# Kernel optimization log

Hardware: AMD Instinct MI355X
Metric: run time of the kernel (lower is better)

Reference implementation:

```python
import jax, jax.numpy as jnp
import numpy as np
from jax import lax

EPS = 1e-5

def haar_dwt(x):
    # pywt 'haar' dwt2: a=(x0+x1)/sqrt2, d=(x0-x1)/sqrt2 per axis
    B, C, H, W = x.shape
    xr = x.reshape(B, C, H // 2, 2, W // 2, 2)
    x00 = xr[:, :, :, 0, :, 0]; x01 = xr[:, :, :, 0, :, 1]
    x10 = xr[:, :, :, 1, :, 0]; x11 = xr[:, :, :, 1, :, 1]
    ll = (x00 + x01 + x10 + x11) * 0.5
    lh = (x00 + x01 - x10 - x11) * 0.5  # cH: detail along rows
    hl = (x00 - x01 + x10 - x11) * 0.5  # cV: detail along cols
    hh = (x00 - x01 - x10 + x11) * 0.5  # cD
    return ll, lh, hl, hh

def haar_idwt(ll, lh, hl, hh):
    y00 = (ll + lh + hl + hh) * 0.5
    y01 = (ll + lh - hl - hh) * 0.5
    y10 = (ll - lh + hl - hh) * 0.5
    y11 = (ll - lh - hl + hh) * 0.5
    B, C, H, W = ll.shape
    top = jnp.stack([y00, y01], axis=-1)      # [B,C,H,W,2]
    bot = jnp.stack([y10, y11], axis=-1)
    y = jnp.stack([top, bot], axis=3)          # [B,C,H,2,W,2]
    return y.reshape(B, C, 2 * H, 2 * W)

def conv1x1(x, w, b):
    # w: [Cout, Cin]
    return jnp.einsum('bchw,oc->bohw', x, w) + b[None, :, None, None]

def batchnorm(x, g, b):
    mu = jnp.mean(x, axis=(0, 2, 3), keepdims=True)
    var = jnp.var(x, axis=(0, 2, 3), keepdims=True)
    xh = (x - mu) * lax.rsqrt(var + EPS)
    return xh * g[None, :, None, None] + b[None, :, None, None]

def layernorm_chw(x, g, b):
    # GroupNorm(1, C): normalize over (C,H,W) per sample
    mu = jnp.mean(x, axis=(1, 2, 3), keepdims=True)
    var = jnp.var(x, axis=(1, 2, 3), keepdims=True)
    xh = (x - mu) * lax.rsqrt(var + EPS)
    return xh * g[None, :, None, None] + b[None, :, None, None]

def dwconv3x3(x, w, b):
    # w: [C,1,3,3] depthwise
    C = x.shape[1]
    y = lax.conv_general_dilated(x, w, (1, 1), [(1, 1), (1, 1)],
                                 dimension_numbers=('NCHW', 'OIHW', 'NCHW'),
                                 feature_group_count=C)
    return y + b[None, :, None, None]

gelu = lambda x: jax.nn.gelu(x, approximate=False)

def setup_inputs() -> dict:
    key = jax.random.key(0)
    ks = jax.random.split(key, 16)
    C = 128
    B, H, W = 8, 256, 256
    f = jnp.float32
    s = lambda k, shape, fan: jax.random.normal(k, shape, f) * (1.0 / np.sqrt(fan))
    return {
        'x': jax.random.normal(ks[0], (B, C, H, W), f),
        'w_c1': s(ks[1], (C, 4 * C), 4 * C), 'b_c1': jnp.zeros((C,), f),
        'bn1_g': jnp.ones((C,), f), 'bn1_b': jnp.zeros((C,), f),
        'dw_w': s(ks[2], (C, 1, 3, 3), 9), 'dw_b': jnp.zeros((C,), f),
        'gn_g': jnp.ones((C,), f), 'gn_b': jnp.zeros((C,), f),
        'pw1_w': s(ks[3], (C, C), C), 'pw1_b': jnp.zeros((C,), f),
        'pw2_w': s(ks[4], (C, C), C), 'pw2_b': jnp.zeros((C,), f),
        'w_c2': s(ks[5], (4 * C, C), C), 'b_c2': jnp.zeros((4 * C,), f),
        'bn2_g': jnp.ones((4 * C,), f), 'bn2_b': jnp.zeros((4 * C,), f),
    }

def reference(x, w_c1, b_c1, bn1_g, bn1_b, dw_w, dw_b, gn_g, gn_b,
              pw1_w, pw1_b, pw2_w, pw2_b, w_c2, b_c2, bn2_g, bn2_b):
    ll, lh, hl, hh = haar_dwt(x)
    h = jnp.concatenate([ll, lh, hl, hh], axis=1)       # [B,4C,H/2,W/2]
    h = gelu(batchnorm(conv1x1(h, w_c1, b_c1), bn1_g, bn1_b))
    # BasicBlock
    res = h
    o = dwconv3x3(h, dw_w, dw_b)
    o = layernorm_chw(o, gn_g, gn_b)
    o = conv1x1(o, pw1_w, pw1_b)
    o = gelu(o)
    o = conv1x1(o, pw2_w, pw2_b)
    h = o + res
    h = gelu(batchnorm(conv1x1(h, w_c2, b_c2), bn2_g, bn2_b))
    C = h.shape[1] // 4
    return haar_idwt(h[:, :C], h[:, C:2 * C], h[:, 2 * C:3 * C], h[:, 3 * C:])
```

## Files before the change

kernel.cpp:

```cpp
#include <hip/hip_runtime.h>
#include <hip/hip_bf16.h>

typedef unsigned short u16;
typedef unsigned int u32;
typedef __attribute__((ext_vector_type(8))) short short8;
typedef __attribute__((ext_vector_type(4))) float f32x4;

#define Bq 8
#define Cc 128
#define C4 512
#define Hh 256
#define Wf 256
#define H2 128
#define W2 128
#define HW2 16384
#define NPIX 131072.0f

__device__ __forceinline__ float gelu_f(float x) {
    float u = 1.5957691216057308f * (x + 0.044715f * x * x * x);
    float t = 1.0f - 2.0f / (__expf(u) + 1.0f);
    return 0.5f * x * (1.0f + t);
}
__device__ __forceinline__ float bf2f(u16 u) {
    union { float f; u32 i; } v; v.i = ((u32)u) << 16; return v.f;
}
__device__ __forceinline__ u16 f2bf(float f) {
    union { float f; u32 i; } v; v.f = f;
    u32 r = v.i + 0x7FFFu + ((v.i >> 16) & 1u);
    return (u16)(r >> 16);
}

__global__ __launch_bounds__(256) void k_wconv(const float* __restrict__ w_c1,
                                               const float* __restrict__ pw1,
                                               const float* __restrict__ pw2,
                                               const float* __restrict__ w_c2,
                                               const float* __restrict__ gn_g,
                                               u16* __restrict__ wb) {
    int i = blockIdx.x * 256 + threadIdx.x;
    float v;
    if (i < 65536) {
        int o = i >> 9, kn = i & 511;
        int c = kn >> 2, dy = (kn >> 1) & 1, dx = kn & 1;
        float sdy = dy ? -1.f : 1.f, sdx = dx ? -1.f : 1.f;
        const float* wr = w_c1 + o * 512 + c;
        v = 0.5f * (wr[0] + sdy * wr[128] + sdx * wr[256] + sdy * sdx * wr[384]);
    } else if (i < 81920) v = pw1[i - 65536] * gn_g[(i - 65536) & 127];
    else if (i < 98304) v = pw2[i - 81920];
    else v = w_c2[i - 98304];
    wb[i] = f2bf(v);
}

__global__ __launch_bounds__(128) void k_wvec(const float* __restrict__ pw1,
                                              const float* __restrict__ gg,
                                              const float* __restrict__ gb,
                                              float* __restrict__ wbv,
                                              float* __restrict__ wgs) {
    int o = threadIdx.x;
    float a = 0.f, bv = 0.f;
    for (int c = 0; c < 128; ++c) {
        float w = pw1[o * 128 + c];
        a += w * gg[c];
        bv += w * gb[c];
    }
    wgs[o] = a;
    wbv[o] = bv;
}

__global__ __launch_bounds__(512) void k_conv1(const float* __restrict__ x,
                                               const u16* __restrict__ Wt,
                                               u16* __restrict__ Cout,
                                               float* __restrict__ statS,
                                               float* __restrict__ statQ) {
    __shared__ __align__(16) u16 lds[16384];
    __shared__ float sblk[128], qblk[128];
    const int t = threadIdx.x;
    const int lane = t & 63, w = t >> 6, wr = w & 1, wc = w >> 1;
    const int b = blockIdx.z, i = blockIdx.y;
    if (t < 128) { sblk[t] = 0.f; qblk[t] = 0.f; }

    const int r15 = lane & 15, kq = lane >> 4;
    const int half = t >> 8;
    const int colblk = t & 7, cc = (t >> 3) & 15, dy = (t >> 7) & 1;
    const int kbase = cc * 4 + dy * 2;
    const int gG = kbase >> 3, e2 = (kbase & 7) * 2;

    float4 xv[4];
    uint4 rb[2];
    {
        const float* xp = x + (((long)(b * Cc + cc)) * Hh + (2 * i + dy)) * Wf;
#pragma unroll
        for (int q = 0; q < 4; ++q) {
            int col = (half * 4 + q) * 32 + colblk * 4;
            xv[q] = *(const float4*)(xp + col);
        }
#pragma unroll
        for (int ii = 0; ii < 2; ++ii) {
            int s = ii * 512 + t;
            rb[ii] = *(const uint4*)(Wt + (long)(s >> 3) * 512 + (s & 7) * 8);
        }
    }

    f32x4 acc[4][2];
#pragma unroll
    for (int a2 = 0; a2 < 4; ++a2)
#pragma unroll
        for (int j2 = 0; j2 < 2; ++j2) acc[a2][j2] = (f32x4){0.f, 0.f, 0.f, 0.f};

    for (int k0 = 0; k0 < 512; k0 += 64) {
        __syncthreads();
#pragma unroll
        for (int q = 0; q < 4; ++q) {
            int col = (half * 4 + q) * 32 + colblk * 4;
            int j0 = col >> 1;
            u32 p0 = (u32)f2bf(xv[q].x) | ((u32)f2bf(xv[q].y) << 16);
            u32 p1 = (u32)f2bf(xv[q].z) | ((u32)f2bf(xv[q].w) << 16);
            *(u32*)((char*)lds + j0 * 128 + 16 * (gG ^ (j0 & 7)) + e2) = p0;
            *(u32*)((char*)lds + (j0 + 1) * 128 + 16 * (gG ^ ((j0 + 1) & 7)) + e2) = p1;
        }
#pragma unroll
        for (int ii = 0; ii < 2; ++ii) {
            int s = ii * 512 + t;
            int row_ = s >> 3, ch_ = s & 7;
            *(uint4*)((char*)lds + 16384 + row_ * 128 + 16 * (ch_ ^ (row_ & 7))) = rb[ii];
        }
        __syncthreads();
        if (k0 + 64 < 512) {
            const int c0n = (k0 + 64) >> 2;
            const float* xp = x + (((long)(b * Cc + c0n + cc)) * Hh + (2 * i + dy)) * Wf;
#pragma unroll
            for (int q = 0; q < 4; ++q) {
                int col = (half * 4 + q) * 32 + colblk * 4;
                xv[q] = *(const float4*)(xp + col);
            }
#pragma unroll
            for (int ii = 0; ii < 2; ++ii) {
                int s = ii * 512 + t;
                rb[ii] = *(const uint4*)(Wt + (long)(s >> 3) * 512 + (k0 + 64) + (s & 7) * 8);
            }
        }
#pragma unroll
        for (int ks = 0; ks < 2; ++ks) {
            short8 af[4], bfv[2];
            const int ch = ks * 4 + kq;
#pragma unroll
            for (int mi = 0; mi < 4; ++mi) {
                int row = wr * 64 + mi * 16 + r15;
                af[mi] = *(const short8*)((const char*)lds + row * 128 + 16 * (ch ^ (row & 7)));
            }
#pragma unroll
            for (int ni = 0; ni < 2; ++ni) {
                int row = wc * 32 + ni * 16 + r15;
                bfv[ni] = *(const short8*)((const char*)lds + 16384 + row * 128 + 16 * (ch ^ (row & 7)));
            }
#pragma unroll
            for (int mi = 0; mi < 4; ++mi)
#pragma unroll
                for (int ni = 0; ni < 2; ++ni)
                    acc[mi][ni] = __builtin_amdgcn_mfma_f32_16x16x32_bf16(
                        af[mi], bfv[ni], acc[mi][ni], 0, 0, 0);
        }
    }
    __syncthreads();

#pragma unroll
    for (int mi = 0; mi < 4; ++mi)
#pragma unroll
        for (int ni = 0; ni < 2; ++ni)
#pragma unroll
            for (int r = 0; r < 4; ++r) {
                int row = wr * 64 + mi * 16 + kq * 4 + r;
                int col = wc * 32 + ni * 16 + r15;
                lds[row * 128 + (col ^ ((row & 7) << 3))] = f2bf(acc[mi][ni][r]);
            }
#pragma unroll
    for (int ni = 0; ni < 2; ++ni) {
        float s = 0.f, q2 = 0.f;
#pragma unroll
        for (int mi = 0; mi < 4; ++mi)
#pragma unroll
            for (int r = 0; r < 4; ++r) {
                float v = acc[mi][ni][r];
                s += v; q2 += v * v;
            }
        s += __shfl_down(s, 32); s += __shfl_down(s, 16);
        q2 += __shfl_down(q2, 32); q2 += __shfl_down(q2, 16);
        if (lane < 16) {
            int col = wc * 32 + ni * 16 + r15;
            atomicAdd(&sblk[col], s);
            atomicAdd(&qblk[col], q2);
        }
    }
    __syncthreads();
    {
        u16* Cb = Cout + (long)b * HW2 * 128;
        int row = t >> 2, quarter = (t & 3) * 32;
        int sx = (row & 7) << 3;
        long gbase = (long)(i * 128 + row) * 128;
#pragma unroll
        for (int q = 0; q < 4; ++q) {
            int c = quarter + q * 8;
            *(uint4*)(Cb + gbase + c) = *(const uint4*)(lds + row * 128 + (c ^ sx));
        }
    }
    if (t < 128) {
        atomicAdd(statS + (long)t * 16, sblk[t]);
        atomicAdd(statQ + (long)t * 16, qblk[t]);
    }
}

__global__ __launch_bounds__(256) void k_bn1_gelu(const u16* __restrict__ in,
                                                  u16* __restrict__ out,
                                                  const float* __restrict__ sum,
                                                  const float* __restrict__ sq,
                                                  const float* __restrict__ g,
                                                  const float* __restrict__ bb) {
    long e = ((long)blockIdx.x * 256 + threadIdx.x) * 8;
    int c0 = (int)(e & 127);
    uint4 raw = *(const uint4*)(in + e);
    u16* pv = (u16*)&raw;
    const float invN = 1.0f / 131072.0f;
#pragma unroll
    for (int u = 0; u < 8; ++u) {
        int c = c0 + u;
        float mu = sum[(long)c * 16] * invN;
        float var = sq[(long)c * 16] * invN - mu * mu;
        float rscale = rsqrtf(var + 1e-5f);
        float sc = rscale * g[c], sh = bb[c] - mu * sc;
        pv[u] = f2bf(gelu_f(bf2f(pv[u]) * sc + sh));
    }
    *(uint4*)(out + e) = raw;
}

__global__ __launch_bounds__(256) void k_dwconv(const u16* __restrict__ x,
                                                u16* __restrict__ y,
                                                const float* __restrict__ w,
                                                const float* __restrict__ bias,
                                                float* __restrict__ lnS,
                                                float* __restrict__ lnQ) {
    __shared__ float wl2[1152];
    const int t = threadIdx.x;
    for (int idx = t; idx < 1152; idx += 256) {
        int c = idx / 9, tap = idx - c * 9;
        wl2[tap * 128 + (c & 7) * 16 + (c >> 3)] = w[idx];
    }
    __syncthreads();
    const int cg = t & 15, jj = t >> 4;
    const int j = blockIdx.x * 16 + jj, i = blockIdx.y, b = blockIdx.z;
    const u16* xb = x + (long)b * HW2 * 128 + cg * 8;
    uint4 raw[3][3];
    const uint4 z4 = make_uint4(0u, 0u, 0u, 0u);
#pragma unroll
    for (int r = 0; r < 3; ++r) {
        int row = i - 1 + r;
#pragma unroll
        for (int q = 0; q < 3; ++q) {
            int col = j - 1 + q;
            bool ok = (row >= 0) & (row < H2) & (col >= 0) & (col < W2);
            raw[r][q] = ok ? *(const uint4*)(xb + ((long)row * W2 + col) * 128) : z4;
        }
    }
    float acc[8];
#pragma unroll
    for (int u = 0; u < 8; ++u) acc[u] = bias[cg * 8 + u];
#pragma unroll
    for (int r = 0; r < 3; ++r)
#pragma unroll
        for (int q = 0; q < 3; ++q) {
            const u16* pv = (const u16*)&raw[r][q];
            const int tap = r * 3 + q;
#pragma unroll
            for (int u = 0; u < 8; ++u)
                acc[u] = fmaf(bf2f(pv[u]), wl2[tap * 128 + u * 16 + cg], acc[u]);
        }
    uint4 outv; u16* ov = (u16*)&outv;
    float s = 0.f, q2 = 0.f;
#pragma unroll
    for (int u = 0; u < 8; ++u) {
        ov[u] = f2bf(acc[u]);
        s += acc[u]; q2 += acc[u] * acc[u];
    }
    *(uint4*)(y + ((long)b * HW2 + (long)i * W2 + j) * 128 + cg * 8) = outv;
#pragma unroll
    for (int off = 32; off; off >>= 1) {
        s += __shfl_down(s, off);
        q2 += __shfl_down(q2, off);
    }
    __shared__ float r1[4], r2[4];
    if ((t & 63) == 0) { r1[t >> 6] = s; r2[t >> 6] = q2; }
    __syncthreads();
    if (t == 0) {
        int slot = (blockIdx.y * 8 + blockIdx.x) & 63;
        atomicAdd(lnS + ((long)b * 64 + slot) * 16, r1[0] + r1[1] + r1[2] + r1[3]);
        atomicAdd(lnQ + ((long)b * 64 + slot) * 16, r2[0] + r2[1] + r2[2] + r2[3]);
    }
}

__global__ __launch_bounds__(256) void k_mlp(const u16* __restrict__ D,
                                             const u16* __restrict__ Wp1,
                                             const u16* __restrict__ Wp2,
                                             const float* __restrict__ b1,
                                             const float* __restrict__ b2,
                                             const u16* __restrict__ resH,
                                             u16* __restrict__ Yout,
                                             const float* __restrict__ lnS,
                                             const float* __restrict__ lnQ,
                                             const float* __restrict__ wbv,
                                             const float* __restrict__ wgs) {
    __shared__ __align__(16) u16 lA[16384];
    __shared__ __align__(16) u16 lB[16384];
    __shared__ float s1[128], s2[128], lnred[2];
    const int t = threadIdx.x;
    const int lane = t & 63, w = t >> 6, wr = w >> 1, wc = w & 1;
    const int r15 = lane & 15, kq = lane >> 4;
    const int b = blockIdx.z, m0 = blockIdx.y * 128;

    if (t < 64) {
        float s = lnS[((long)b * 64 + t) * 16];
        float q = lnQ[((long)b * 64 + t) * 16];
#pragma unroll
        for (int off = 32; off; off >>= 1) {
            s += __shfl_down(s, off);
            q += __shfl_down(q, off);
        }
        if (t == 0) { lnred[0] = s; lnred[1] = q; }
    }
    __syncthreads();
    const float invN = 1.0f / 2097152.0f;
    float mu = lnred[0] * invN;
    float var = lnred[1] * invN - mu * mu;
    const float rs = rsqrtf(var + 1e-5f);
    if (t < 128) {
        s1[t] = b1[t] + wbv[t] - mu * rs * wgs[t];
        s2[t] = b2[t];
    }

    const u16* Ab = D + ((long)b * HW2 + m0) * 128;
    uint4 ga[8], gb[8];
#pragma unroll
    for (int i = 0; i < 8; ++i) {
        int s = i * 256 + t, row = s >> 4, seg = s & 15;
        ga[i] = *(const uint4*)(Ab + (long)row * 128 + seg * 8);
        gb[i] = *(const uint4*)(Wp1 + (long)row * 128 + seg * 8);
    }
#pragma unroll
    for (int i = 0; i < 8; ++i) {
        int s = i * 256 + t, row = s >> 4, seg = s & 15;
        int off = (seg >> 3) * 16384 + row * 128 + 16 * ((seg & 7) ^ (row & 7));
        *(uint4*)((char*)lA + off) = ga[i];
        *(uint4*)((char*)lB + off) = gb[i];
    }
    __syncthreads();

    f32x4 acc[4][4];
#pragma unroll
    for (int i = 0; i < 4; ++i)
#pragma unroll
        for (int j = 0; j < 4; ++j) acc[i][j] = (f32x4){0.f, 0.f, 0.f, 0.f};
#pragma unroll
    for (int chunk = 0; chunk < 2; ++chunk)
#pragma unroll
        for (int ks = 0; ks < 2; ++ks) {
            const int ch = ks * 4 + kq;
            short8 af[4], bfv[4];
#pragma unroll
            for (int mi = 0; mi < 4; ++mi) {
                int row = wr * 64 + mi * 16 + r15;
                af[mi] = *(const short8*)((const char*)lA + chunk * 16384 +
                                          row * 128 + 16 * (ch ^ (row & 7)));
            }
#pragma unroll
            for (int ni = 0; ni < 4; ++ni) {
                int row = wc * 64 + ni * 16 + r15;
                bfv[ni] = *(const short8*)((const char*)lB + chunk * 16384 +
                                           row * 128 + 16 * (ch ^ (row & 7)));
            }
#pragma unroll
            for (int mi = 0; mi < 4; ++mi)
#pragma unroll
                for (int ni = 0; ni < 4; ++ni)
                    acc[mi][ni] = __builtin_amdgcn_mfma_f32_16x16x32_bf16(
                        af[mi], bfv[ni], acc[mi][ni], 0, 0, 0);
        }
#pragma unroll
    for (int i = 0; i < 8; ++i) {
        int s = i * 256 + t, row = s >> 4, seg = s & 15;
        gb[i] = *(const uint4*)(Wp2 + (long)row * 128 + seg * 8);
    }
    __syncthreads();

#pragma unroll
    for (int mi = 0; mi < 4; ++mi)
#pragma unroll
        for (int ni = 0; ni < 4; ++ni)
#pragma unroll
            for (int r = 0; r < 4; ++r) {
                int row = wr * 64 + mi * 16 + kq * 4 + r;
                int col = wc * 64 + ni * 16 + r15;
                float v = gelu_f(rs * acc[mi][ni][r] + s1[col]);
                lA[(col >> 6) * 8192 + row * 64 +
                   8 * (((col >> 3) & 7) ^ (row & 7)) + (col & 7)] = f2bf(v);
            }
#pragma unroll
    for (int i = 0; i < 8; ++i) {
        int s = i * 256 + t, row = s >> 4, seg = s & 15;
        int off = (seg >> 3) * 16384 + row * 128 + 16 * ((seg & 7) ^ (row & 7));
        *(uint4*)((char*)lB + off) = gb[i];
    }
    __syncthreads();

#pragma unroll
    for (int i = 0; i < 4; ++i)
#pragma unroll
        for (int j = 0; j < 4; ++j) acc[i][j] = (f32x4){0.f, 0.f, 0.f, 0.f};
#pragma unroll
    for (int chunk = 0; chunk < 2; ++chunk)
#pragma unroll
        for (int ks = 0; ks < 2; ++ks) {
            const int ch = ks * 4 + kq;
            short8 af[4], bfv[4];
#pragma unroll
            for (int mi = 0; mi < 4; ++mi) {
                int row = wr * 64 + mi * 16 + r15;
                af[mi] = *(const short8*)((const char*)lA + chunk * 16384 +
                                          row * 128 + 16 * (ch ^ (row & 7)));
            }
#pragma unroll
            for (int ni = 0; ni < 4; ++ni) {
                int row = wc * 64 + ni * 16 + r15;
                bfv[ni] = *(const short8*)((const char*)lB + chunk * 16384 +
                                           row * 128 + 16 * (ch ^ (row & 7)));
            }
#pragma unroll
            for (int mi = 0; mi < 4; ++mi)
#pragma unroll
                for (int ni = 0; ni < 4; ++ni)
                    acc[mi][ni] = __builtin_amdgcn_mfma_f32_16x16x32_bf16(
                        af[mi], bfv[ni], acc[mi][ni], 0, 0, 0);
        }
    __syncthreads();

#pragma unroll
    for (int mi = 0; mi < 4; ++mi)
#pragma unroll
        for (int ni = 0; ni < 4; ++ni)
#pragma unroll
            for (int r = 0; r < 4; ++r) {
                int row = wr * 64 + mi * 16 + kq * 4 + r;
                int col = wc * 64 + ni * 16 + r15;
                lA[row * 128 + (col ^ ((row & 7) << 3))] = f2bf(acc[mi][ni][r]);
            }
    __syncthreads();

    const u16* Rb = resH + ((long)b * HW2 + m0) * 128;
    u16* Cb = Yout + ((long)b * HW2 + m0) * 128;
    {
        int row = t >> 1, half = (t & 1) * 64;
        int sx = (row & 7) << 3;
#pragma unroll
        for (int q = 0; q < 8; ++q) {
            int c = half + q * 8;
            uint4 raw = *(const uint4*)(lA + row * 128 + (c ^ sx));
            uint4 rr = *(const uint4*)(Rb + (long)row * 128 + c);
            u16* pv = (u16*)&raw;
            const u16* rv = (const u16*)&rr;
#pragma unroll
            for (int u = 0; u < 8; ++u)
                pv[u] = f2bf(bf2f(pv[u]) + s2[c + u] + bf2f(rv[u]));
            *(uint4*)(Cb + (long)row * 128 + c) = raw;
        }
    }
}

__global__ __launch_bounds__(256) void k_moment(const u16* __restrict__ Y,
                                                float* __restrict__ M2,
                                                float* __restrict__ csum) {
    __shared__ __align__(16) u16 T[8192];
    __shared__ float cred[16][16][8];
    const int t = threadIdx.x;
    const int lane = t & 63, w = t >> 6, wr = w >> 1, wc = w & 1;
    const int r15 = lane & 15, kq = lane >> 4;
    const long px0 = (long)blockIdx.x * 1024;
    float cs[8] = {};

    f32x4 acc[4][4];
#pragma unroll
    for (int i = 0; i < 4; ++i)
#pragma unroll
        for (int j = 0; j < 4; ++j) acc[i][j] = (f32x4){0.f, 0.f, 0.f, 0.f};

    for (int it = 0; it < 16; ++it) {
        uint4 rv[4];
#pragma unroll
        for (int i = 0; i < 4; ++i) {
            int s = i * 256 + t;
            int px = s >> 4, ch8 = (s & 15) * 8;
            rv[i] = *(const uint4*)(Y + (px0 + it * 64 + px) * 128 + ch8);
        }
#pragma unroll
        for (int i = 0; i < 4; ++i) {
            const u16* pv = (const u16*)&rv[i];
#pragma unroll
            for (int u = 0; u < 8; ++u) cs[u] += bf2f(pv[u]);
        }
        __syncthreads();
#pragma unroll
        for (int i = 0; i < 4; ++i) {
            int s = i * 256 + t;
            int px = s >> 4, ch8 = (s & 15) * 8;
            const u16* pv = (const u16*)&rv[i];
#pragma unroll
            for (int u = 0; u < 8; ++u) {
                int row = ch8 + u;
                T[row * 64 + 8 * ((px >> 3) ^ (row & 7)) + (px & 7)] = pv[u];
            }
        }
        __syncthreads();
#pragma unroll
        for (int ks = 0; ks < 2; ++ks) {
            const int ch = ks * 4 + kq;
            short8 af[4], bfv[4];
#pragma unroll
            for (int mi = 0; mi < 4; ++mi) {
                int row = wr * 64 + mi * 16 + r15;
                af[mi] = *(const short8*)(T + row * 64 + 8 * (ch ^ (row & 7)));
            }
#pragma unroll
            for (int ni = 0; ni < 4; ++ni) {
                int row = wc * 64 + ni * 16 + r15;
                bfv[ni] = *(const short8*)(T + row * 64 + 8 * (ch ^ (row & 7)));
            }
#pragma unroll
            for (int mi = 0; mi < 4; ++mi)
#pragma unroll
                for (int ni = 0; ni < 4; ++ni)
                    acc[mi][ni] = __builtin_amdgcn_mfma_f32_16x16x32_bf16(
                        af[mi], bfv[ni], acc[mi][ni], 0, 0, 0);
        }
    }
    {
        int g = t & 15, m = t >> 4;
#pragma unroll
        for (int u = 0; u < 8; ++u) cred[m][g][u] = cs[u];
    }
    __syncthreads();
    if (t < 128) {
        float s = 0.f;
#pragma unroll
        for (int m = 0; m < 16; ++m) s += cred[m][t >> 3][t & 7];
        atomicAdd(csum + (long)t * 16, s);
    }
#pragma unroll
    for (int mi = 0; mi < 4; ++mi)
#pragma unroll
        for (int ni = 0; ni < 4; ++ni)
#pragma unroll
            for (int r = 0; r < 4; ++r) {
                int row = wr * 64 + mi * 16 + kq * 4 + r;
                int col = wc * 64 + ni * 16 + r15;
                atomicAdd(M2 + row * 128 + col, acc[mi][ni][r]);
            }
}

__global__ __launch_bounds__(128) void k_statcomb(const float* __restrict__ w_c2,
                                                  const float* __restrict__ M2,
                                                  const float* __restrict__ csum,
                                                  const float* __restrict__ g,
                                                  const float* __restrict__ bb,
                                                  float* __restrict__ scsh) {
    __shared__ float wl[128];
    __shared__ float red[2][2];
    const int o = blockIdx.x, c = threadIdx.x;
    wl[c] = w_c2[o * 128 + c];
    __syncthreads();
    const float* m2r = M2 + c * 128;
    float tmp = 0.f;
#pragma unroll
    for (int c2 = 0; c2 < 128; c2 += 4) {
        float4 m = *(const float4*)(m2r + c2);
        tmp += m.x * wl[c2] + m.y * wl[c2 + 1] + m.z * wl[c2 + 2] + m.w * wl[c2 + 3];
    }
    float s2p = wl[c] * tmp;
    float mup = wl[c] * csum[(long)c * 16];
#pragma unroll
    for (int off = 32; off; off >>= 1) {
        s2p += __shfl_down(s2p, off);
        mup += __shfl_down(mup, off);
    }
    if ((c & 63) == 0) { red[0][c >> 6] = s2p; red[1][c >> 6] = mup; }
    __syncthreads();
    if (c == 0) {
        float s2 = (red[0][0] + red[0][1]) / NPIX;
        float mu = (red[1][0] + red[1][1]) / NPIX;
        float var = s2 - mu * mu;
        float rs = rsqrtf(var + 1e-5f);
        float sc = g[o] * rs;
        scsh[o] = sc;
        scsh[512 + o] = bb[o] - mu * sc;
    }
}

__global__ __launch_bounds__(512) void k_conv2_idwt(const u16* __restrict__ Y,
                                                    const u16* __restrict__ Wc,
                                                    const float* __restrict__ scsh,
                                                    float* __restrict__ out) {
    __shared__ __align__(16) u16 lA[16384];
    __shared__ __align__(16) u16 lB[8192];
    __shared__ float sparam[1024];
    const int t = threadIdx.x;
    const int lane = t & 63, w = t >> 6, wr = w & 1, wc = w >> 1;
    const int r15 = lane & 15, kq = lane >> 4;
    const int b = blockIdx.y, n0 = blockIdx.x;
#pragma unroll
    for (int u = 0; u < 2; ++u) sparam[t + u * 512] = scsh[t + u * 512];

    const u16* Yb = Y + ((long)b * HW2 + (long)n0 * 64) * 128;
    uint4 rb2[2], ra4[4];
#pragma unroll
    for (int i = 0; i < 2; ++i) {
        int s = i * 512 + t, row = s >> 4, seg = s & 15;
        rb2[i] = *(const uint4*)(Yb + (long)row * 128 + seg * 8);
    }
#define GLOADA(q)                                                                \
    {                                                                            \
        _Pragma("unroll")                                                        \
        for (int i = 0; i < 4; ++i) {                                            \
            int s = i * 512 + t, row = s >> 4, seg = s & 15;                     \
            ra4[i] = *(const uint4*)(Wc + (long)((q) * 128 + row) * 128 + seg * 8); \
        }                                                                        \
    }
#define LWRITEA()                                                                \
    {                                                                            \
        _Pragma("unroll")                                                        \
        for (int i = 0; i < 4; ++i) {                                            \
            int s = i * 512 + t, row = s >> 4, seg = s & 15;                     \
            *(uint4*)((char*)lA + (seg >> 3) * 16384 + row * 128 +               \
                      16 * ((seg & 7) ^ (row & 7))) = ra4[i];                    \
        }                                                                        \
    }
    GLOADA(0)
#pragma unroll
    for (int i = 0; i < 2; ++i) {
        int s = i * 512 + t, row = s >> 4, seg = s & 15;
        *(uint4*)((char*)lB + (seg >> 3) * 8192 + row * 128 +
                  16 * ((seg & 7) ^ (row & 7))) = rb2[i];
    }
    LWRITEA()
    __syncthreads();

    u32 sbp[4][4][2];
#pragma unroll
    for (int q = 0; q < 4; ++q) {
        f32x4 acc[4];
#pragma unroll
        for (int mi = 0; mi < 4; ++mi) acc[mi] = (f32x4){0.f, 0.f, 0.f, 0.f};
#pragma unroll
        for (int chunk = 0; chunk < 2; ++chunk)
#pragma unroll
            for (int ks = 0; ks < 2; ++ks) {
                const int ch = ks * 4 + kq;
                short8 af[4], bfv;
#pragma unroll
                for (int mi = 0; mi < 4; ++mi) {
                    int row = wr * 64 + mi * 16 + r15;
                    af[mi] = *(const short8*)((const char*)lA + chunk * 16384 +
                                              row * 128 + 16 * (ch ^ (row & 7)));
                }
                {
                    int row = wc * 16 + r15;
                    bfv = *(const short8*)((const char*)lB + chunk * 8192 +
                                           row * 128 + 16 * (ch ^ (row & 7)));
                }
#pragma unroll
                for (int mi = 0; mi < 4; ++mi)
                    acc[mi] = __builtin_amdgcn_mfma_f32_16x16x32_bf16(
                        af[mi], bfv, acc[mi], 0, 0, 0);
            }
        if (q < 3) GLOADA(q + 1)
#pragma unroll
        for (int mi = 0; mi < 4; ++mi)
#pragma unroll
            for (int rp = 0; rp < 2; ++rp) {
                int c0 = q * 128 + wr * 64 + mi * 16 + kq * 4 + rp * 2;
                float v0 = gelu_f(acc[mi][rp * 2] * sparam[c0] + sparam[512 + c0]);
                float v1 = gelu_f(acc[mi][rp * 2 + 1] * sparam[c0 + 1] + sparam[512 + c0 + 1]);
                sbp[q][mi][rp] = (u32)f2bf(v0) | ((u32)f2bf(v1) << 16);
            }
        if (q < 3) {
            __syncthreads();
            LWRITEA()
            __syncthreads();
        }
    }
    const int i = n0 >> 1;
    const int j = (n0 & 1) * 64 + wc * 16 + r15;
#pragma unroll
    for (int mi = 0; mi < 4; ++mi)
#pragma unroll
        for (int rp = 0; rp < 2; ++rp) {
            u32 p0 = sbp[0][mi][rp], p1 = sbp[1][mi][rp];
            u32 p2 = sbp[2][mi][rp], p3 = sbp[3][mi][rp];
#pragma unroll
            for (int e = 0; e < 2; ++e) {
                int c = wr * 64 + mi * 16 + kq * 4 + rp * 2 + e;
                float ll = bf2f(e ? (u16)(p0 >> 16) : (u16)(p0 & 0xFFFF));
                float lh = bf2f(e ? (u16)(p1 >> 16) : (u16)(p1 & 0xFFFF));
                float hl = bf2f(e ? (u16)(p2 >> 16) : (u16)(p2 & 0xFFFF));
                float hh = bf2f(e ? (u16)(p3 >> 16) : (u16)(p3 & 0xFFFF));
                long ob = (((long)(b * Cc + c) * Hh + 2 * i) * Wf + 2 * j);
                *(float2*)(out + ob) =
                    make_float2((ll + lh + hl + hh) * 0.5f, (ll + lh - hl - hh) * 0.5f);
                *(float2*)(out + ob + Wf) =
                    make_float2((ll - lh + hl - hh) * 0.5f, (ll - lh - hl + hh) * 0.5f);
            }
        }
#undef GLOADA
#undef LWRITEA
}

extern "C" void kernel_launch(void* const* d_in, const int* in_sizes, int n_in,
                              void* d_out, int out_size, void* d_ws, size_t ws_size,
                              hipStream_t stream) {
    const float* x     = (const float*)d_in[0];
    const float* w_c1  = (const float*)d_in[1];
    const float* bn1_g = (const float*)d_in[3];
    const float* bn1_b = (const float*)d_in[4];
    const float* dw_w  = (const float*)d_in[5];
    const float* dw_b  = (const float*)d_in[6];
    const float* gn_g  = (const float*)d_in[7];
    const float* gn_b  = (const float*)d_in[8];
    const float* pw1_w = (const float*)d_in[9];
    const float* pw1_b = (const float*)d_in[10];
    const float* pw2_w = (const float*)d_in[11];
    const float* pw2_b = (const float*)d_in[12];
    const float* w_c2  = (const float*)d_in[13];
    const float* bn2_g = (const float*)d_in[15];
    const float* bn2_b = (const float*)d_in[16];
    float* out = (float*)d_out;

    const size_t n128 = (size_t)Bq * Cc * HW2;
    u16* bufA = (u16*)d_ws;
    u16* bufH = bufA + n128;
    u16* bufD = bufH + n128;
    u16* bufY = bufD + n128;
    u16* wb   = bufY + n128;
    float* stats = (float*)(wb + 163840);
    size_t need = (4 * n128 + 163840) * 2 + 41000 * 4;
    if (ws_size < need) return;

    float* bn1_sum = stats;
    float* bn1_sq  = stats + 2048;
    float* ln_sum  = stats + 4096;
    float* ln_sq   = stats + 12288;
    float* csum    = stats + 20480;
    float* M2      = stats + 22528;
    float* scsh    = stats + 38912;
    float* wbv     = stats + 39936;
    float* wgs     = stats + 40064;

    hipMemsetAsync(stats, 0, 38912 * sizeof(float), stream);

    k_wconv<<<640, 256, 0, stream>>>(w_c1, pw1_w, pw2_w, w_c2, gn_g, wb);
    k_wvec<<<1, 128, 0, stream>>>(pw1_w, gn_g, gn_b, wbv, wgs);

    k_conv1<<<dim3(1, 128, 8), 512, 0, stream>>>(x, wb, bufA, bn1_sum, bn1_sq);

    k_bn1_gelu<<<8192, 256, 0, stream>>>(bufA, bufH, bn1_sum, bn1_sq, bn1_g, bn1_b);

    k_dwconv<<<dim3(8, 128, 8), 256, 0, stream>>>(bufH, bufD, dw_w, dw_b, ln_sum, ln_sq);

    k_mlp<<<dim3(1, 128, 8), 256, 0, stream>>>(
        bufD, wb + 65536, wb + 81920, pw1_b, pw2_b, bufH, bufY,
        ln_sum, ln_sq, wbv, wgs);

    k_moment<<<128, 256, 0, stream>>>(bufY, M2, csum);
    k_statcomb<<<512, 128, 0, stream>>>(w_c2, M2, csum, bn2_g, bn2_b, scsh);

    k_conv2_idwt<<<dim3(256, 8), 512, 0, stream>>>(bufY, wb + 98304, scsh, out);
}
```

Baseline: 476.5 us.

## Fuse BN1+GELU into dwconv and MLP residual; replace M2 atomics with partial reduction

Removes the standalone BN1+GELU pass. The depthwise conv now stages a halo tile in LDS and applies the BN scale/shift plus GELU while loading it. The MLP kernel recomputes GELU(BN(x)) for its residual input, which removes one full bf16 tensor write and read. The moment kernel now writes per-block partial Gram matrices, and a new reduction kernel sums them instead of issuing global float atomics. The costs are recomputed GELU work, a larger workspace for the partials (about 8 MB), and an extra kernel launch.

```diff
diff --git a/kernel.cpp b/kernel.cpp
--- a/kernel.cpp
+++ b/kernel.cpp
@@ -208,69 +208,73 @@
     }
 }
 
-__global__ __launch_bounds__(256) void k_bn1_gelu(const u16* __restrict__ in,
-                                                  u16* __restrict__ out,
-                                                  const float* __restrict__ sum,
-                                                  const float* __restrict__ sq,
-                                                  const float* __restrict__ g,
-                                                  const float* __restrict__ bb) {
-    long e = ((long)blockIdx.x * 256 + threadIdx.x) * 8;
-    int c0 = (int)(e & 127);
-    uint4 raw = *(const uint4*)(in + e);
-    u16* pv = (u16*)&raw;
-    const float invN = 1.0f / 131072.0f;
-#pragma unroll
-    for (int u = 0; u < 8; ++u) {
-        int c = c0 + u;
-        float mu = sum[(long)c * 16] * invN;
-        float var = sq[(long)c * 16] * invN - mu * mu;
-        float rscale = rsqrtf(var + 1e-5f);
-        float sc = rscale * g[c], sh = bb[c] - mu * sc;
-        pv[u] = f2bf(gelu_f(bf2f(pv[u]) * sc + sh));
-    }
-    *(uint4*)(out + e) = raw;
-}
-
-__global__ __launch_bounds__(256) void k_dwconv(const u16* __restrict__ x,
+__global__ __launch_bounds__(256) void k_dwconv(const u16* __restrict__ xin,
                                                 u16* __restrict__ y,
                                                 const float* __restrict__ w,
                                                 const float* __restrict__ bias,
+                                                const float* __restrict__ bnS,
+                                                const float* __restrict__ bnQ,
+                                                const float* __restrict__ g1,
+                                                const float* __restrict__ b1,
                                                 float* __restrict__ lnS,
                                                 float* __restrict__ lnQ) {
     __shared__ float wl2[1152];
+    __shared__ float sA[128], sB[128];
+    __shared__ __align__(16) u16 tile[3 * 18 * 136];
     const int t = threadIdx.x;
+    if (t < 128) {
+        const float invN = 1.0f / 131072.0f;
+        float mu = bnS[(long)t * 16] * invN;
+        float var = bnQ[(long)t * 16] * invN - mu * mu;
+        float rs = rsqrtf(var + 1e-5f);
+        float sc = rs * g1[t];
+        sA[t] = sc;
+        sB[t] = b1[t] - mu * sc;
+    }
     for (int idx = t; idx < 1152; idx += 256) {
         int c = idx / 9, tap = idx - c * 9;
         wl2[tap * 128 + (c & 7) * 16 + (c >> 3)] = w[idx];
     }
     __syncthreads();
+    const int jbase = blockIdx.x * 16, i = blockIdx.y, b = blockIdx.z;
+    const u16* xb = xin + (long)b * HW2 * 128;
+    {
+        int seg = t & 15, slot0 = t >> 4;
+#pragma unroll
+        for (int pass = 0; pass < 4; ++pass) {
+            int slot = pass * 16 + slot0;
+            if (slot < 54) {
+                int r = slot / 18, p = slot - r * 18;
+                int row = i - 1 + r, col = jbase - 1 + p;
+                bool inb = (row >= 0) & (row < H2) & (col >= 0) & (col < W2);
+                uint4 raw = inb ? *(const uint4*)(xb + ((long)row * W2 + col) * 128 + seg * 8)
+                                : make_uint4(0u, 0u, 0u, 0u);
+                const u16* pv = (const u16*)&raw;
+                uint4 outv; u16* ov = (u16*)&outv;
+#pragma unroll
+                for (int u = 0; u < 8; ++u) {
+                    int c = seg * 8 + u;
+                    float v = inb ? gelu_f(bf2f(pv[u]) * sA[c] + sB[c]) : 0.f;
+                    ov[u] = f2bf(v);
+                }
+                *(uint4*)(tile + slot * 136 + seg * 8) = outv;
+            }
+        }
+    }
+    __syncthreads();
     const int cg = t & 15, jj = t >> 4;
-    const int j = blockIdx.x * 16 + jj, i = blockIdx.y, b = blockIdx.z;
-    const u16* xb = x + (long)b * HW2 * 128 + cg * 8;
-    uint4 raw[3][3];
-    const uint4 z4 = make_uint4(0u, 0u, 0u, 0u);
-#pragma unroll
-    for (int r = 0; r < 3; ++r) {
-        int row = i - 1 + r;
-#pragma unroll
-        for (int q = 0; q < 3; ++q) {
-            int col = j - 1 + q;
-            bool ok = (row >= 0) & (row < H2) & (col >= 0) & (col < W2);
-            raw[r][q] = ok ? *(const uint4*)(xb + ((long)row * W2 + col) * 128) : z4;
-        }
-    }
     float acc[8];
 #pragma unroll
     for (int u = 0; u < 8; ++u) acc[u] = bias[cg * 8 + u];
 #pragma unroll
     for (int r = 0; r < 3; ++r)
 #pragma unroll
-        for (int q = 0; q < 3; ++q) {
-            const u16* pv = (const u16*)&raw[r][q];
-            const int tap = r * 3 + q;
+        for (int dj = 0; dj < 3; ++dj) {
+            short8 vv = *(const short8*)(tile + (r * 18 + jj + dj) * 136 + cg * 8);
+            const int tap = r * 3 + dj;
 #pragma unroll
             for (int u = 0; u < 8; ++u)
-                acc[u] = fmaf(bf2f(pv[u]), wl2[tap * 128 + u * 16 + cg], acc[u]);
+                acc[u] = fmaf(bf2f((u16)vv[u]), wl2[tap * 128 + u * 16 + cg], acc[u]);
         }
     uint4 outv; u16* ov = (u16*)&outv;
     float s = 0.f, q2 = 0.f;
@@ -279,7 +283,7 @@
         ov[u] = f2bf(acc[u]);
         s += acc[u]; q2 += acc[u] * acc[u];
     }
-    *(uint4*)(y + ((long)b * HW2 + (long)i * W2 + j) * 128 + cg * 8) = outv;
+    *(uint4*)(y + ((long)b * HW2 + (long)i * W2 + jbase + jj) * 128 + cg * 8) = outv;
 #pragma unroll
     for (int off = 32; off; off >>= 1) {
         s += __shfl_down(s, off);
@@ -298,17 +302,21 @@
 __global__ __launch_bounds__(256) void k_mlp(const u16* __restrict__ D,
                                              const u16* __restrict__ Wp1,
                                              const u16* __restrict__ Wp2,
-                                             const float* __restrict__ b1,
-                                             const float* __restrict__ b2,
-                                             const u16* __restrict__ resH,
+                                             const float* __restrict__ b1p,
+                                             const float* __restrict__ b2p,
+                                             const u16* __restrict__ resA,
                                              u16* __restrict__ Yout,
                                              const float* __restrict__ lnS,
                                              const float* __restrict__ lnQ,
                                              const float* __restrict__ wbv,
-                                             const float* __restrict__ wgs) {
+                                             const float* __restrict__ wgs,
+                                             const float* __restrict__ bnS,
+                                             const float* __restrict__ bnQ,
+                                             const float* __restrict__ g1,
+                                             const float* __restrict__ b1v) {
     __shared__ __align__(16) u16 lA[16384];
     __shared__ __align__(16) u16 lB[16384];
-    __shared__ float s1[128], s2[128], lnred[2];
+    __shared__ float s1[128], s2[128], sA[128], sB[128], lnred[2];
     const int t = threadIdx.x;
     const int lane = t & 63, w = t >> 6, wr = w >> 1, wc = w & 1;
     const int r15 = lane & 15, kq = lane >> 4;
@@ -330,8 +338,15 @@
     float var = lnred[1] * invN - mu * mu;
     const float rs = rsqrtf(var + 1e-5f);
     if (t < 128) {
-        s1[t] = b1[t] + wbv[t] - mu * rs * wgs[t];
-        s2[t] = b2[t];
+        s1[t] = b1p[t] + wbv[t] - mu * rs * wgs[t];
+        s2[t] = b2p[t];
+        const float invN1 = 1.0f / 131072.0f;
+        float mu1 = bnS[(long)t * 16] * invN1;
+        float var1 = bnQ[(long)t * 16] * invN1 - mu1 * mu1;
+        float rs1 = rsqrtf(var1 + 1e-5f);
+        float sc1 = rs1 * g1[t];
+        sA[t] = sc1;
+        sB[t] = b1v[t] - mu1 * sc1;
     }
 
     const u16* Ab = D + ((long)b * HW2 + m0) * 128;
@@ -451,7 +466,7 @@
             }
     __syncthreads();
 
-    const u16* Rb = resH + ((long)b * HW2 + m0) * 128;
+    const u16* Ra = resA + ((long)b * HW2 + m0) * 128;
     u16* Cb = Yout + ((long)b * HW2 + m0) * 128;
     {
         int row = t >> 1, half = (t & 1) * 64;
@@ -460,19 +475,21 @@
         for (int q = 0; q < 8; ++q) {
             int c = half + q * 8;
             uint4 raw = *(const uint4*)(lA + row * 128 + (c ^ sx));
-            uint4 rr = *(const uint4*)(Rb + (long)row * 128 + c);
+            uint4 rr = *(const uint4*)(Ra + (long)row * 128 + c);
             u16* pv = (u16*)&raw;
             const u16* rv = (const u16*)&rr;
 #pragma unroll
-            for (int u = 0; u < 8; ++u)
-                pv[u] = f2bf(bf2f(pv[u]) + s2[c + u] + bf2f(rv[u]));
+            for (int u = 0; u < 8; ++u) {
+                float hres = gelu_f(bf2f(rv[u]) * sA[c + u] + sB[c + u]);
+                pv[u] = f2bf(bf2f(pv[u]) + s2[c + u] + hres);
+            }
             *(uint4*)(Cb + (long)row * 128 + c) = raw;
         }
     }
 }
 
 __global__ __launch_bounds__(256) void k_moment(const u16* __restrict__ Y,
-                                                float* __restrict__ M2,
+                                                float* __restrict__ M2p,
                                                 float* __restrict__ csum) {
     __shared__ __align__(16) u16 T[8192];
     __shared__ float cred[16][16][8];
@@ -549,6 +566,7 @@
         for (int m = 0; m < 16; ++m) s += cred[m][t >> 3][t & 7];
         atomicAdd(csum + (long)t * 16, s);
     }
+    float* Mb = M2p + (long)blockIdx.x * 16384;
 #pragma unroll
     for (int mi = 0; mi < 4; ++mi)
 #pragma unroll
@@ -557,8 +575,16 @@
             for (int r = 0; r < 4; ++r) {
                 int row = wr * 64 + mi * 16 + kq * 4 + r;
                 int col = wc * 64 + ni * 16 + r15;
-                atomicAdd(M2 + row * 128 + col, acc[mi][ni][r]);
-            }
+                Mb[row * 128 + col] = acc[mi][ni][r];
+            }
+}
+
+__global__ __launch_bounds__(256) void k_m2red(const float* __restrict__ M2p,
+                                               float* __restrict__ M2) {
+    int e = blockIdx.x * 256 + threadIdx.x;
+    float s = 0.f;
+    for (int p = 0; p < 128; ++p) s += M2p[(long)p * 16384 + e];
+    M2[e] = s;
 }
 
 __global__ __launch_bounds__(128) void k_statcomb(const float* __restrict__ w_c2,
@@ -739,12 +765,12 @@
 
     const size_t n128 = (size_t)Bq * Cc * HW2;
     u16* bufA = (u16*)d_ws;
-    u16* bufH = bufA + n128;
-    u16* bufD = bufH + n128;
+    u16* bufD = bufA + n128;
     u16* bufY = bufD + n128;
     u16* wb   = bufY + n128;
     float* stats = (float*)(wb + 163840);
-    size_t need = (4 * n128 + 163840) * 2 + 41000 * 4;
+    float* M2p = stats + 49152;
+    size_t need = (3 * n128 + 163840) * 2 + (49152 + 128 * 16384) * 4;
     if (ws_size < need) return;
 
     float* bn1_sum = stats;
@@ -757,22 +783,23 @@
     float* wbv     = stats + 39936;
     float* wgs     = stats + 40064;
 
-    hipMemsetAsync(stats, 0, 38912 * sizeof(float), stream);
+    hipMemsetAsync(stats, 0, 22528 * sizeof(float), stream);
 
     k_wconv<<<640, 256, 0, stream>>>(w_c1, pw1_w, pw2_w, w_c2, gn_g, wb);
     k_wvec<<<1, 128, 0, stream>>>(pw1_w, gn_g, gn_b, wbv, wgs);
 
     k_conv1<<<dim3(1, 128, 8), 512, 0, stream>>>(x, wb, bufA, bn1_sum, bn1_sq);
 
-    k_bn1_gelu<<<8192, 256, 0, stream>>>(bufA, bufH, bn1_sum, bn1_sq, bn1_g, bn1_b);
-
-    k_dwconv<<<dim3(8, 128, 8), 256, 0, stream>>>(bufH, bufD, dw_w, dw_b, ln_sum, ln_sq);
+    k_dwconv<<<dim3(8, 128, 8), 256, 0, stream>>>(bufA, bufD, dw_w, dw_b,
+                                                  bn1_sum, bn1_sq, bn1_g, bn1_b,
+                                                  ln_sum, ln_sq);
 
     k_mlp<<<dim3(1, 128, 8), 256, 0, stream>>>(
-        bufD, wb + 65536, wb + 81920, pw1_b, pw2_b, bufH, bufY,
-        ln_sum, ln_sq, wbv, wgs);
-
-    k_moment<<<128, 256, 0, stream>>>(bufY, M2, csum);
+        bufD, wb + 65536, wb + 81920, pw1_b, pw2_b, bufA, bufY,
+        ln_sum, ln_sq, wbv, wgs, bn1_sum, bn1_sq, bn1_g, bn1_b);
+
+    k_moment<<<128, 256, 0, stream>>>(bufY, M2p, csum);
+    k_m2red<<<64, 256, 0, stream>>>(M2p, M2);
     k_statcomb<<<512, 128, 0, stream>>>(w_c2, M2, csum, bn2_g, bn2_b, scsh);
 
     k_conv2_idwt<<<dim3(256, 8), 512, 0, stream>>>(bufY, wb + 98304, scsh, out);
```

New measurement: 423.5 us. 11.1% less time.
